# Performance work log

Measured on AMD Instinct MI355X. Metric: run time of the kernel, lower is better.

## Reference

```python
import jax, jax.numpy as jnp
import numpy as np

D_MODEL = 2048
NUM_HEADS = 16
HEAD_DIM = D_MODEL // NUM_HEADS


def _rotary(x, head_dim):
    # x: (..., T, head_dim). Matches torch module: half-split rotation.
    T = x.shape[-2]
    pos = jnp.arange(T, dtype=jnp.float32)[:, None]              # (T,1)
    dim = jnp.arange(head_dim // 2, dtype=jnp.float32)[None, :]  # (1,hd/2)
    angle = pos * (1.0 / jnp.power(10000.0, 2.0 * dim / head_dim))
    cos = jnp.cos(angle)  # (T, hd/2), broadcasts over leading dims
    sin = jnp.sin(angle)
    x1 = x[..., : head_dim // 2]
    x2 = x[..., head_dim // 2:]
    return jnp.concatenate([x1 * cos - x2 * sin, x2 * cos + x1 * sin], axis=-1)


def setup_inputs() -> dict:
    key = jax.random.key(0)
    ks = jax.random.split(key, 9)
    B, T, D, H, HD = 2, 2048, D_MODEL, NUM_HEADS, HEAD_DIM
    s = 1.0 / np.sqrt(D)
    return {
        "x": jax.random.normal(ks[0], (B, T, D), jnp.float32),
        "Wq": jax.random.normal(ks[1], (D, D), jnp.float32) * s,
        "bq": jnp.zeros((D,), jnp.float32),
        "Wk": jax.random.normal(ks[2], (D, HD), jnp.float32) * s,
        "bk": jnp.zeros((HD,), jnp.float32),
        "Wv": jax.random.normal(ks[3], (D, HD), jnp.float32) * s,
        "bv": jnp.zeros((HD,), jnp.float32),
        "Wo": jax.random.normal(ks[4], (D, D), jnp.float32) * s,
        "bo": jnp.zeros((D,), jnp.float32),
    }


def reference(x, Wq, bq, Wk, bk, Wv, bv, Wo, bo):
    B, T, D = x.shape
    H, HD = NUM_HEADS, HEAD_DIM
    q = (x @ Wq + bq).reshape(B, T, H, HD).transpose(0, 2, 1, 3)  # (B,H,T,hd)
    k = (x @ Wk + bk)[:, None]                                    # (B,1,T,hd)
    v = (x @ Wv + bv)[:, None]                                    # (B,1,T,hd)
    q = _rotary(q, HD)
    k = _rotary(k, HD)
    scores = jnp.einsum("bhqd,bhkd->bhqk", q, jnp.broadcast_to(k, (B, 1, T, HD))) / jnp.sqrt(jnp.float32(HD))
    attn = jax.nn.softmax(scores, axis=-1)                        # (B,H,T,T)
    ctx = jnp.einsum("bhqk,bhkd->bhqd", attn, jnp.broadcast_to(v, (B, 1, T, HD)))
    ctx = ctx.transpose(0, 2, 1, 3).reshape(B, T, D)
    return ctx @ Wo + bo
```

## Files before the change

### kernel.cpp

```cpp
#include <hip/hip_runtime.h>
#include <math.h>

#define T_SEQ  2048
#define DMODEL 2048
#define NHEADS 16
#define HDIM   128
#define MROWS  4096

typedef __attribute__((ext_vector_type(8)))  __bf16 bf16x8;
typedef __attribute__((ext_vector_type(4)))  __bf16 bf16x4;
typedef __attribute__((ext_vector_type(4)))  float  f32x4;
typedef __attribute__((ext_vector_type(16))) float  f32x16;

#define GLOBAL_AS __attribute__((address_space(1)))
#define LDS_AS    __attribute__((address_space(3)))
__device__ __forceinline__ void async_copy16(const __bf16* g, __bf16* l) {
  __builtin_amdgcn_global_load_lds((const GLOBAL_AS void*)g, (LDS_AS void*)l, 16, 0, 0);
}

__global__ void build_rope_kernel(float2* __restrict__ rope) {
  int idx = blockIdx.x * blockDim.x + threadIdx.x;
  int d = idx & 63, pos = idx >> 6;
  double freq = pow(10000.0, -(double)d / 64.0);
  double ang = (double)pos * freq;
  rope[idx] = make_float2((float)cos(ang), (float)sin(ang));
}

__global__ void cast_bf16_kernel(const float* __restrict__ in,
                                 __bf16* __restrict__ out, int n4) {
  int i = blockIdx.x * blockDim.x + threadIdx.x;
  if (i >= n4) return;
  float4 v = ((const float4*)in)[i];
  bf16x4 o = { (__bf16)v.x, (__bf16)v.y, (__bf16)v.z, (__bf16)v.w };
  *(bf16x4*)(out + (size_t)i*4) = o;
}

__global__ void wtrans_kernel(const float* __restrict__ Wq,
                              const float* __restrict__ Wk,
                              const float* __restrict__ Wv,
                              const float* __restrict__ Wo,
                              __bf16* __restrict__ wqkvt,
                              __bf16* __restrict__ wot) {
  __shared__ float t[32][33];
  const int bx = blockIdx.x;
  const float* src; __bf16* dst; int istride, c0, orow;
  if (bx < 64)       { src = Wq; istride = 2048; c0 = bx*32;      orow = c0;        dst = wqkvt; }
  else if (bx < 68)  { src = Wk; istride = 128;  c0 = (bx-64)*32; orow = 2048 + c0; dst = wqkvt; }
  else if (bx < 72)  { src = Wv; istride = 128;  c0 = (bx-68)*32; orow = 2176 + c0; dst = wqkvt; }
  else               { src = Wo; istride = 2048; c0 = (bx-72)*32; orow = c0;        dst = wot; }
  const int tx = threadIdx.x & 31, ty = threadIdx.x >> 5;
  const int r0 = blockIdx.y*32;
#pragma unroll
  for (int i = 0; i < 4; ++i)
    t[ty + i*8][tx] = src[(size_t)(r0 + ty + i*8)*istride + c0 + tx];
  __syncthreads();
#pragma unroll
  for (int i = 0; i < 4; ++i)
    dst[(size_t)(orow + ty + i*8)*2048 + r0 + tx] = (__bf16)t[tx][ty + i*8];
}

__global__ void transpose_v_kernel(const __bf16* __restrict__ in,
                                   __bf16* __restrict__ out) {
  __shared__ __bf16 t[32][34];
  const int bz = blockIdx.z;
  in  += (size_t)bz * 2048 * 128;
  out += (size_t)bz * 128 * 2048;
  const int tx = threadIdx.x & 31, ty = threadIdx.x >> 5;
  const int r0 = blockIdx.y*32, c0 = blockIdx.x*32;
#pragma unroll
  for (int i = 0; i < 4; ++i)
    t[ty + i*8][tx] = in[(size_t)(r0 + ty + i*8)*128 + c0 + tx];
  __syncthreads();
#pragma unroll
  for (int i = 0; i < 4; ++i)
    out[(size_t)(c0 + ty + i*8)*2048 + r0 + tx] = t[tx][ty + i*8];
}

__global__ __launch_bounds__(256) void gemm_qkv_fused(
    const __bf16* __restrict__ A,
    const __bf16* __restrict__ Bt,
    const float* __restrict__ bq, const float* __restrict__ bk,
    const float* __restrict__ bv,
    const float2* __restrict__ rope,
    __bf16* __restrict__ qrb,
    __bf16* __restrict__ kbb,
    __bf16* __restrict__ vbb,
    float qscale)
{
  __shared__ __bf16 As[128*32];
  __shared__ __bf16 Bs[128*32];
  const int tid = threadIdx.x;
  const int lane = tid & 63, wave = tid >> 6;
  const int quad = lane >> 4, l16 = lane & 15;
  const int m0 = (wave >> 1)*64, n0 = (wave & 1)*32;
  const int row0 = blockIdx.y*128, col0 = blockIdx.x*128;
  const int srow = lane >> 2, scol = (lane & 3)*8;

  f32x4 acc[4][4];
#pragma unroll
  for (int i = 0; i < 4; ++i)
#pragma unroll
    for (int j = 0; j < 4; ++j) acc[i][j] = (f32x4){0.f,0.f,0.f,0.f};

  const __bf16* Ag = A  + (size_t)(row0 + wave*32 + srow)*DMODEL + scol;
  const __bf16* Bg = Bt + (size_t)(col0 + wave*32 + srow)*DMODEL + scol;
  __bf16* AsW = &As[wave*1024];
  __bf16* BsW = &Bs[wave*1024];

  for (int kk = 0; kk < DMODEL; kk += 32) {
    __syncthreads();
    async_copy16(Ag + kk,                     AsW);
    async_copy16(Ag + kk + (size_t)16*DMODEL, AsW + 512);
    async_copy16(Bg + kk,                     BsW);
    async_copy16(Bg + kk + (size_t)16*DMODEL, BsW + 512);
    __syncthreads();
    bf16x8 af[4], bfr[4];
#pragma unroll
    for (int i = 0; i < 4; ++i)
      af[i] = *(const bf16x8*)&As[(m0 + i*16 + l16)*32 + quad*8];
#pragma unroll
    for (int j = 0; j < 4; ++j) {
      const int cb = n0 + (j & 1)*16 + (j >> 1)*64;
      bfr[j] = *(const bf16x8*)&Bs[(cb + l16)*32 + quad*8];
    }
#pragma unroll
    for (int i = 0; i < 4; ++i)
#pragma unroll
      for (int j = 0; j < 4; ++j)
        acc[i][j] = __builtin_amdgcn_mfma_f32_16x16x32_bf16(af[i], bfr[j], acc[i][j], 0,0,0);
  }

  const int bx = blockIdx.x;
  const float* bias_p; float scale; bool rot; __bf16* obase; int ostride;
  if (bx < 16)      { bias_p = bq + bx*128; scale = qscale; rot = true;
                      obase = qrb + bx*128; ostride = 2048; }
  else if (bx == 16){ bias_p = bk; scale = 1.f; rot = true;
                      obase = kbb; ostride = 128; }
  else              { bias_p = bv; scale = 1.f; rot = false;
                      obase = vbb; ostride = 128; }

#pragma unroll
  for (int j = 0; j < 2; ++j) {
    const int d = n0 + j*16 + l16;
    const float b1 = bias_p[d], b2 = bias_p[d + 64];
#pragma unroll
    for (int i = 0; i < 4; ++i) {
      const int rl = m0 + i*16 + quad*4;
#pragma unroll
      for (int r = 0; r < 4; ++r) {
        const int rg = row0 + rl + r;
        const float x1 = acc[i][j][r]   + b1;
        const float x2 = acc[i][j+2][r] + b2;
        float c = 1.f, s = 0.f;
        if (rot) { float2 cs = rope[(size_t)(rg & (T_SEQ-1))*64 + d]; c = cs.x; s = cs.y; }
        obase[(size_t)rg*ostride + d]      = (__bf16)((x1*c - x2*s)*scale);
        obase[(size_t)rg*ostride + d + 64] = (__bf16)((x2*c + x1*s)*scale);
      }
    }
  }
}

__global__ __launch_bounds__(256) void gemm_bf16_t128(
    const __bf16* __restrict__ A, const __bf16* __restrict__ Bt,
    const float* __restrict__ bias, float* __restrict__ C,
    int M, int N, int K)
{
  __shared__ __bf16 As[128*32];
  __shared__ __bf16 Bs[128*32];
  const int tid = threadIdx.x;
  const int lane = tid & 63, wave = tid >> 6;
  const int quad = lane >> 4, l16 = lane & 15;
  const int m0 = (wave & 1)*64, n0 = (wave >> 1)*64;
  const int row0 = blockIdx.y*128, col0 = blockIdx.x*128;
  const int srow = lane >> 2, scol = (lane & 3)*8;

  f32x4 acc[4][4];
#pragma unroll
  for (int i = 0; i < 4; ++i)
#pragma unroll
    for (int j = 0; j < 4; ++j) acc[i][j] = (f32x4){0.f,0.f,0.f,0.f};

  const __bf16* Ag = A  + (size_t)(row0 + wave*32 + srow)*K + scol;
  const __bf16* Bg = Bt + (size_t)(col0 + wave*32 + srow)*K + scol;
  __bf16* AsW = &As[wave*1024];
  __bf16* BsW = &Bs[wave*1024];

  for (int kk = 0; kk < K; kk += 32) {
    __syncthreads();
    async_copy16(Ag + kk,              AsW);
    async_copy16(Ag + kk + (size_t)16*K, AsW + 512);
    async_copy16(Bg + kk,              BsW);
    async_copy16(Bg + kk + (size_t)16*K, BsW + 512);
    __syncthreads();
    bf16x8 af[4], bfr[4];
#pragma unroll
    for (int i = 0; i < 4; ++i)
      af[i] = *(const bf16x8*)&As[(m0 + i*16 + l16)*32 + quad*8];
#pragma unroll
    for (int j = 0; j < 4; ++j)
      bfr[j] = *(const bf16x8*)&Bs[(n0 + j*16 + l16)*32 + quad*8];
#pragma unroll
    for (int i = 0; i < 4; ++i)
#pragma unroll
      for (int j = 0; j < 4; ++j)
        acc[i][j] = __builtin_amdgcn_mfma_f32_16x16x32_bf16(af[i], bfr[j], acc[i][j], 0,0,0);
  }
#pragma unroll
  for (int j = 0; j < 4; ++j) {
    const int ccol = col0 + n0 + j*16 + l16;
    const float bvv = bias[ccol];
#pragma unroll
    for (int i = 0; i < 4; ++i) {
      const int crow = row0 + m0 + i*16 + quad*4;
#pragma unroll
      for (int r = 0; r < 4; ++r)
        C[(size_t)(crow + r)*N + ccol] = acc[i][j][r] + bvv;
    }
  }
}

#define KSTR 136
#define VSTR 72
__global__ __launch_bounds__(256) void mqa_attn_mfma(
    const __bf16* __restrict__ qb,
    const __bf16* __restrict__ kb,
    const __bf16* __restrict__ vt,
    __bf16* __restrict__ ctx)
{
  __shared__ __bf16 Ks[64*KSTR];
  __shared__ __bf16 Vs[128*VSTR];
  const int tid = threadIdx.x, lane = tid & 63, wave = tid >> 6;
  const int h5 = lane >> 5, l32 = lane & 31;
  const int swr = (l32 & 19) | ((l32 & 4) << 1) | ((l32 & 8) >> 1);
  const int h = blockIdx.y, b = blockIdx.z;
  const int qbase = blockIdx.x*128 + wave*32;

  bf16x8 qf[8];
  const __bf16* qp = qb + ((size_t)b*T_SEQ + qbase + l32)*DMODEL + h*HDIM;
#pragma unroll
  for (int ds = 0; ds < 8; ++ds) qf[ds] = *(const bf16x8*)(qp + ds*16 + h5*8);

  f32x16 oacc[4];
#pragma unroll
  for (int g = 0; g < 4; ++g)
#pragma unroll
    for (int r = 0; r < 16; ++r) oacc[g][r] = 0.f;
  float lsum = 0.f;

  const __bf16* kbase = kb + (size_t)b*T_SEQ*HDIM;
  const __bf16* vbase = vt + (size_t)b*HDIM*T_SEQ;

  const int kkey = tid >> 2;
  const int kcol = (tid & 3)*32;

  bf16x8 kreg[4], vreg[4];
#pragma unroll
  for (int i = 0; i < 4; ++i) {
    int idx = i*256 + tid;
    kreg[i] = *(const bf16x8*)(kbase + (size_t)(idx >> 4)*HDIM + (idx & 15)*8);
    vreg[i] = *(const bf16x8*)(vbase + (size_t)(idx >> 3)*T_SEQ + (idx & 7)*8);
  }

  constexpr int NT = T_SEQ/64;
  for (int kt = 0; kt < NT; ++kt) {
    __syncthreads();
#pragma unroll
    for (int i = 0; i < 4; ++i) {
      int idx = i*256 + tid;
      *(bf16x8*)&Ks[(idx >> 4)*KSTR + (idx & 15)*8] = kreg[i];
      *(bf16x8*)&Vs[(idx >> 3)*VSTR + (idx & 7)*8]  = vreg[i];
    }
    __syncthreads();
    {
      const int ktn = (kt + 1 < NT) ? kt + 1 : 0;
#pragma unroll
      for (int i = 0; i < 4; ++i) {
        int idx = i*256 + tid;
        kreg[i] = *(const bf16x8*)(kbase + (size_t)(ktn*64 + (idx >> 4))*HDIM + (idx & 15)*8);
        vreg[i] = *(const bf16x8*)(vbase + (size_t)(idx >> 3)*T_SEQ + ktn*64 + (idx & 7)*8);
      }
    }

    f32x16 s_lo[2], s_hi[2];
#pragma unroll
    for (int kg = 0; kg < 2; ++kg)
#pragma unroll
      for (int r = 0; r < 16; ++r) { s_lo[kg][r] = 0.f; s_hi[kg][r] = 0.f; }
#pragma unroll
    for (int ds = 0; ds < 4; ++ds) {
      bf16x8 k00 = *(const bf16x8*)&Ks[swr*KSTR        + ds*16 + h5*8];
      bf16x8 k01 = *(const bf16x8*)&Ks[(32+swr)*KSTR   + ds*16 + h5*8];
      bf16x8 k10 = *(const bf16x8*)&Ks[swr*KSTR        + (ds+4)*16 + h5*8];
      bf16x8 k11 = *(const bf16x8*)&Ks[(32+swr)*KSTR   + (ds+4)*16 + h5*8];
      s_lo[0] = __builtin_amdgcn_mfma_f32_32x32x16_bf16(k00, qf[ds],   s_lo[0], 0,0,0);
      s_lo[1] = __builtin_amdgcn_mfma_f32_32x32x16_bf16(k01, qf[ds],   s_lo[1], 0,0,0);
      s_hi[0] = __builtin_amdgcn_mfma_f32_32x32x16_bf16(k10, qf[ds+4], s_hi[0], 0,0,0);
      s_hi[1] = __builtin_amdgcn_mfma_f32_32x32x16_bf16(k11, qf[ds+4], s_hi[1], 0,0,0);
    }

    bf16x8 pf[2][2];
#pragma unroll
    for (int kg = 0; kg < 2; ++kg)
#pragma unroll
      for (int r = 0; r < 16; ++r) {
        float p = __builtin_amdgcn_exp2f(s_lo[kg][r] + s_hi[kg][r]);
        lsum += p;
        pf[kg][r >> 3][r & 7] = (__bf16)p;
      }

#pragma unroll
    for (int kg = 0; kg < 2; ++kg)
#pragma unroll
      for (int ks = 0; ks < 2; ++ks) {
#pragma unroll
        for (int g = 0; g < 4; ++g) {
          bf16x8 vf = *(const bf16x8*)&Vs[(g*32 + l32)*VSTR + kg*32 + ks*16 + h5*8];
          oacc[g] = __builtin_amdgcn_mfma_f32_32x32x16_bf16(vf, pf[kg][ks], oacc[g], 0,0,0);
        }
      }
  }

  lsum += __shfl_xor(lsum, 32);
  const float inv = 1.f / lsum;

  __bf16* op = ctx + ((size_t)b*T_SEQ + qbase + l32)*DMODEL + h*HDIM;
#pragma unroll
  for (int g = 0; g < 4; ++g)
#pragma unroll
    for (int rq = 0; rq < 4; ++rq) {
      const int d = g*32 + rq*8 + h5*4;
      bf16x4 ov = { (__bf16)(oacc[g][rq*4+0]*inv), (__bf16)(oacc[g][rq*4+1]*inv),
                    (__bf16)(oacc[g][rq*4+2]*inv), (__bf16)(oacc[g][rq*4+3]*inv) };
      *(bf16x4*)&op[d] = ov;
    }
}

extern "C" void kernel_launch(void* const* d_in, const int* in_sizes, int n_in,
                              void* d_out, int out_size, void* d_ws, size_t ws_size,
                              hipStream_t stream) {
  const float* x  = (const float*)d_in[0];
  const float* Wq = (const float*)d_in[1];
  const float* bq = (const float*)d_in[2];
  const float* Wk = (const float*)d_in[3];
  const float* bk = (const float*)d_in[4];
  const float* Wv = (const float*)d_in[5];
  const float* bv = (const float*)d_in[6];
  const float* Wo = (const float*)d_in[7];
  const float* bo = (const float*)d_in[8];
  float* out = (float*)d_out;

  uint8_t* ws = (uint8_t*)d_ws;
  __bf16* qrb  = (__bf16*)(ws);
  __bf16* xb   = (__bf16*)(ws + 16777216);
  __bf16* wqkvt= (__bf16*)(ws + 33554432);
  __bf16* wot  = (__bf16*)(ws + 42991616);
  __bf16* kbb  = (__bf16*)(ws + 51380224);
  __bf16* vbb  = (__bf16*)(ws + 52428800);
  __bf16* vtb  = (__bf16*)(ws + 53477376);
  float2* rope = (float2*)(ws + 54525952);

  const float qscale = 1.4426950408889634f * 0.08838834764831845f;

  build_rope_kernel<<<512, 256, 0, stream>>>(rope);
  wtrans_kernel<<<dim3(136,64), 256, 0, stream>>>(Wq, Wk, Wv, Wo, wqkvt, wot);
  cast_bf16_kernel<<<8192, 256, 0, stream>>>(x, xb, MROWS*DMODEL/4);

  gemm_qkv_fused<<<dim3(18,32), 256, 0, stream>>>(
      xb, wqkvt, bq, bk, bv, rope, qrb, kbb, vbb, qscale);

  transpose_v_kernel<<<dim3(4,64,2), 256, 0, stream>>>(vbb, vtb);

  mqa_attn_mfma<<<dim3(16,16,2), 256, 0, stream>>>(qrb, kbb, vtb, xb);

  gemm_bf16_t128<<<dim3(16,32), 256, 0, stream>>>(xb, wot, bo, out, MROWS, DMODEL, DMODEL);
}
```

Before: 322.4 us.

## Fuse V transpose into QKV GEMM epilogue and double-buffer attention K/V tiles

```diff
diff --git a/kernel.cpp b/kernel.cpp
--- a/kernel.cpp
+++ b/kernel.cpp
@@ -59,23 +59,6 @@
     dst[(size_t)(orow + ty + i*8)*2048 + r0 + tx] = (__bf16)t[tx][ty + i*8];
 }
 
-__global__ void transpose_v_kernel(const __bf16* __restrict__ in,
-                                   __bf16* __restrict__ out) {
-  __shared__ __bf16 t[32][34];
-  const int bz = blockIdx.z;
-  in  += (size_t)bz * 2048 * 128;
-  out += (size_t)bz * 128 * 2048;
-  const int tx = threadIdx.x & 31, ty = threadIdx.x >> 5;
-  const int r0 = blockIdx.y*32, c0 = blockIdx.x*32;
-#pragma unroll
-  for (int i = 0; i < 4; ++i)
-    t[ty + i*8][tx] = in[(size_t)(r0 + ty + i*8)*128 + c0 + tx];
-  __syncthreads();
-#pragma unroll
-  for (int i = 0; i < 4; ++i)
-    out[(size_t)(c0 + ty + i*8)*2048 + r0 + tx] = t[tx][ty + i*8];
-}
-
 __global__ __launch_bounds__(256) void gemm_qkv_fused(
     const __bf16* __restrict__ A,
     const __bf16* __restrict__ Bt,
@@ -84,7 +67,7 @@
     const float2* __restrict__ rope,
     __bf16* __restrict__ qrb,
     __bf16* __restrict__ kbb,
-    __bf16* __restrict__ vbb,
+    __bf16* __restrict__ vtb,
     float qscale)
 {
   __shared__ __bf16 As[128*32];
@@ -131,30 +114,45 @@
   }
 
   const int bx = blockIdx.x;
-  const float* bias_p; float scale; bool rot; __bf16* obase; int ostride;
-  if (bx < 16)      { bias_p = bq + bx*128; scale = qscale; rot = true;
-                      obase = qrb + bx*128; ostride = 2048; }
-  else if (bx == 16){ bias_p = bk; scale = 1.f; rot = true;
-                      obase = kbb; ostride = 128; }
-  else              { bias_p = bv; scale = 1.f; rot = false;
-                      obase = vbb; ostride = 128; }
-
-#pragma unroll
-  for (int j = 0; j < 2; ++j) {
-    const int d = n0 + j*16 + l16;
-    const float b1 = bias_p[d], b2 = bias_p[d + 64];
-#pragma unroll
-    for (int i = 0; i < 4; ++i) {
-      const int rl = m0 + i*16 + quad*4;
-#pragma unroll
-      for (int r = 0; r < 4; ++r) {
-        const int rg = row0 + rl + r;
-        const float x1 = acc[i][j][r]   + b1;
-        const float x2 = acc[i][j+2][r] + b2;
-        float c = 1.f, s = 0.f;
-        if (rot) { float2 cs = rope[(size_t)(rg & (T_SEQ-1))*64 + d]; c = cs.x; s = cs.y; }
-        obase[(size_t)rg*ostride + d]      = (__bf16)((x1*c - x2*s)*scale);
-        obase[(size_t)rg*ostride + d + 64] = (__bf16)((x2*c + x1*s)*scale);
+  if (bx < 17) {
+    const float* bias_p; float scale; __bf16* obase; int ostride;
+    if (bx < 16) { bias_p = bq + bx*128; scale = qscale; obase = qrb + bx*128; ostride = 2048; }
+    else         { bias_p = bk;          scale = 1.f;    obase = kbb;          ostride = 128; }
+#pragma unroll
+    for (int j = 0; j < 2; ++j) {
+      const int d = n0 + j*16 + l16;
+      const float b1 = bias_p[d], b2 = bias_p[d + 64];
+#pragma unroll
+      for (int i = 0; i < 4; ++i) {
+        const int rl = m0 + i*16 + quad*4;
+#pragma unroll
+        for (int r = 0; r < 4; ++r) {
+          const int rg = row0 + rl + r;
+          const float x1 = acc[i][j][r]   + b1;
+          const float x2 = acc[i][j+2][r] + b2;
+          float2 cs = rope[(size_t)(rg & (T_SEQ-1))*64 + d];
+          obase[(size_t)rg*ostride + d]      = (__bf16)((x1*cs.x - x2*cs.y)*scale);
+          obase[(size_t)rg*ostride + d + 64] = (__bf16)((x2*cs.x + x1*cs.y)*scale);
+        }
+      }
+    }
+  } else {
+    const int bb = row0 >> 11;
+    const int tb = row0 & (T_SEQ - 1);
+    __bf16* vb = vtb + (size_t)bb*HDIM*T_SEQ;
+#pragma unroll
+    for (int j = 0; j < 2; ++j) {
+      const int d = n0 + j*16 + l16;
+      const float b1 = bv[d], b2 = bv[d + 64];
+#pragma unroll
+      for (int i = 0; i < 4; ++i) {
+        const int t0 = tb + m0 + i*16 + quad*4;
+        bf16x4 lo = { (__bf16)(acc[i][j][0]+b1),   (__bf16)(acc[i][j][1]+b1),
+                      (__bf16)(acc[i][j][2]+b1),   (__bf16)(acc[i][j][3]+b1) };
+        bf16x4 hi = { (__bf16)(acc[i][j+2][0]+b2), (__bf16)(acc[i][j+2][1]+b2),
+                      (__bf16)(acc[i][j+2][2]+b2), (__bf16)(acc[i][j+2][3]+b2) };
+        *(bf16x4*)&vb[(size_t)d*T_SEQ + t0]        = lo;
+        *(bf16x4*)&vb[(size_t)(d + 64)*T_SEQ + t0] = hi;
       }
     }
   }
@@ -227,8 +225,8 @@
     const __bf16* __restrict__ vt,
     __bf16* __restrict__ ctx)
 {
-  __shared__ __bf16 Ks[64*KSTR];
-  __shared__ __bf16 Vs[128*VSTR];
+  __shared__ __bf16 Ks[2][64*KSTR];
+  __shared__ __bf16 Vs[2][128*VSTR];
   const int tid = threadIdx.x, lane = tid & 63, wave = tid >> 6;
   const int h5 = lane >> 5, l32 = lane & 31;
   const int swr = (l32 & 19) | ((l32 & 4) << 1) | ((l32 & 8) >> 1);
@@ -245,13 +243,10 @@
   for (int g = 0; g < 4; ++g)
 #pragma unroll
     for (int r = 0; r < 16; ++r) oacc[g][r] = 0.f;
-  float lsum = 0.f;
+  float lsum4[4] = {0.f, 0.f, 0.f, 0.f};
 
   const __bf16* kbase = kb + (size_t)b*T_SEQ*HDIM;
   const __bf16* vbase = vt + (size_t)b*HDIM*T_SEQ;
-
-  const int kkey = tid >> 2;
-  const int kcol = (tid & 3)*32;
 
   bf16x8 kreg[4], vreg[4];
 #pragma unroll
@@ -260,24 +255,38 @@
     kreg[i] = *(const bf16x8*)(kbase + (size_t)(idx >> 4)*HDIM + (idx & 15)*8);
     vreg[i] = *(const bf16x8*)(vbase + (size_t)(idx >> 3)*T_SEQ + (idx & 7)*8);
   }
+#pragma unroll
+  for (int i = 0; i < 4; ++i) {
+    int idx = i*256 + tid;
+    *(bf16x8*)&Ks[0][(idx >> 4)*KSTR + (idx & 15)*8] = kreg[i];
+    *(bf16x8*)&Vs[0][(idx >> 3)*VSTR + (idx & 7)*8]  = vreg[i];
+  }
+#pragma unroll
+  for (int i = 0; i < 4; ++i) {
+    int idx = i*256 + tid;
+    kreg[i] = *(const bf16x8*)(kbase + (size_t)(64 + (idx >> 4))*HDIM + (idx & 15)*8);
+    vreg[i] = *(const bf16x8*)(vbase + (size_t)(idx >> 3)*T_SEQ + 64 + (idx & 7)*8);
+  }
+  __syncthreads();
 
   constexpr int NT = T_SEQ/64;
   for (int kt = 0; kt < NT; ++kt) {
-    __syncthreads();
-#pragma unroll
-    for (int i = 0; i < 4; ++i) {
-      int idx = i*256 + tid;
-      *(bf16x8*)&Ks[(idx >> 4)*KSTR + (idx & 15)*8] = kreg[i];
-      *(bf16x8*)&Vs[(idx >> 3)*VSTR + (idx & 7)*8]  = vreg[i];
-    }
-    __syncthreads();
-    {
-      const int ktn = (kt + 1 < NT) ? kt + 1 : 0;
+    const int cur = kt & 1;
+    if (kt + 1 < NT) {
 #pragma unroll
       for (int i = 0; i < 4; ++i) {
         int idx = i*256 + tid;
-        kreg[i] = *(const bf16x8*)(kbase + (size_t)(ktn*64 + (idx >> 4))*HDIM + (idx & 15)*8);
-        vreg[i] = *(const bf16x8*)(vbase + (size_t)(idx >> 3)*T_SEQ + ktn*64 + (idx & 7)*8);
+        *(bf16x8*)&Ks[1^cur][(idx >> 4)*KSTR + (idx & 15)*8] = kreg[i];
+        *(bf16x8*)&Vs[1^cur][(idx >> 3)*VSTR + (idx & 7)*8]  = vreg[i];
+      }
+    }
+    if (kt + 2 < NT) {
+      const int kn = (kt + 2)*64;
+#pragma unroll
+      for (int i = 0; i < 4; ++i) {
+        int idx = i*256 + tid;
+        kreg[i] = *(const bf16x8*)(kbase + (size_t)(kn + (idx >> 4))*HDIM + (idx & 15)*8);
+        vreg[i] = *(const bf16x8*)(vbase + (size_t)(idx >> 3)*T_SEQ + kn + (idx & 7)*8);
       }
     }
 
@@ -288,10 +297,10 @@
       for (int r = 0; r < 16; ++r) { s_lo[kg][r] = 0.f; s_hi[kg][r] = 0.f; }
 #pragma unroll
     for (int ds = 0; ds < 4; ++ds) {
-      bf16x8 k00 = *(const bf16x8*)&Ks[swr*KSTR        + ds*16 + h5*8];
-      bf16x8 k01 = *(const bf16x8*)&Ks[(32+swr)*KSTR   + ds*16 + h5*8];
-      bf16x8 k10 = *(const bf16x8*)&Ks[swr*KSTR        + (ds+4)*16 + h5*8];
-      bf16x8 k11 = *(const bf16x8*)&Ks[(32+swr)*KSTR   + (ds+4)*16 + h5*8];
+      bf16x8 k00 = *(const bf16x8*)&Ks[cur][swr*KSTR      + ds*16 + h5*8];
+      bf16x8 k01 = *(const bf16x8*)&Ks[cur][(32+swr)*KSTR + ds*16 + h5*8];
+      bf16x8 k10 = *(const bf16x8*)&Ks[cur][swr*KSTR      + (ds+4)*16 + h5*8];
+      bf16x8 k11 = *(const bf16x8*)&Ks[cur][(32+swr)*KSTR + (ds+4)*16 + h5*8];
       s_lo[0] = __builtin_amdgcn_mfma_f32_32x32x16_bf16(k00, qf[ds],   s_lo[0], 0,0,0);
       s_lo[1] = __builtin_amdgcn_mfma_f32_32x32x16_bf16(k01, qf[ds],   s_lo[1], 0,0,0);
       s_hi[0] = __builtin_amdgcn_mfma_f32_32x32x16_bf16(k10, qf[ds+4], s_hi[0], 0,0,0);
@@ -304,7 +313,7 @@
 #pragma unroll
       for (int r = 0; r < 16; ++r) {
         float p = __builtin_amdgcn_exp2f(s_lo[kg][r] + s_hi[kg][r]);
-        lsum += p;
+        lsum4[r & 3] += p;
         pf[kg][r >> 3][r & 7] = (__bf16)p;
       }
 
@@ -314,12 +323,14 @@
       for (int ks = 0; ks < 2; ++ks) {
 #pragma unroll
         for (int g = 0; g < 4; ++g) {
-          bf16x8 vf = *(const bf16x8*)&Vs[(g*32 + l32)*VSTR + kg*32 + ks*16 + h5*8];
+          bf16x8 vf = *(const bf16x8*)&Vs[cur][(g*32 + l32)*VSTR + kg*32 + ks*16 + h5*8];
           oacc[g] = __builtin_amdgcn_mfma_f32_32x32x16_bf16(vf, pf[kg][ks], oacc[g], 0,0,0);
         }
       }
-  }
-
+    __syncthreads();
+  }
+
+  float lsum = (lsum4[0] + lsum4[1]) + (lsum4[2] + lsum4[3]);
   lsum += __shfl_xor(lsum, 32);
   const float inv = 1.f / lsum;
 
@@ -355,9 +366,8 @@
   __bf16* wqkvt= (__bf16*)(ws + 33554432);
   __bf16* wot  = (__bf16*)(ws + 42991616);
   __bf16* kbb  = (__bf16*)(ws + 51380224);
-  __bf16* vbb  = (__bf16*)(ws + 52428800);
-  __bf16* vtb  = (__bf16*)(ws + 53477376);
-  float2* rope = (float2*)(ws + 54525952);
+  __bf16* vtb  = (__bf16*)(ws + 52428800);
+  float2* rope = (float2*)(ws + 53477376);
 
   const float qscale = 1.4426950408889634f * 0.08838834764831845f;
 
@@ -366,9 +376,7 @@
   cast_bf16_kernel<<<8192, 256, 0, stream>>>(x, xb, MROWS*DMODEL/4);
 
   gemm_qkv_fused<<<dim3(18,32), 256, 0, stream>>>(
-      xb, wqkvt, bq, bk, bv, rope, qrb, kbb, vbb, qscale);
-
-  transpose_v_kernel<<<dim3(4,64,2), 256, 0, stream>>>(vbb, vtb);
+      xb, wqkvt, bq, bk, bv, rope, qrb, kbb, vtb, qscale);
 
   mqa_attn_mfma<<<dim3(16,16,2), 256, 0, stream>>>(qrb, kbb, vtb, xb);
 
```

Measured after the change: 367.6 us. 1.14x slower.
